# Optimization experiments

Hardware: AMD Instinct MI355X
Metric: run time of the kernel (lower is better)

Reference implementation:

```python
import jax, jax.numpy as jnp
import numpy as np

# Mamba-2 dims (from wrapper: d_model=hidden_size=2048, d_state=64, d_conv=4, expand=2, headdim=64)
D_MODEL = 2048
EXPAND = 2
HEADDIM = 64
D_STATE = 64
D_CONV = 4
D_INNER = EXPAND * D_MODEL            # 4096
NHEADS = D_INNER // HEADDIM           # 64
NGROUPS = 1                           # mamba_ssm default
CONV_DIM = D_INNER + 2 * NGROUPS * D_STATE          # 4224
D_IN_PROJ = 2 * D_INNER + 2 * NGROUPS * D_STATE + NHEADS  # 8384
BATCH = 1
SEQLEN = 1024
RMS_EPS = 1e-5


def setup_inputs() -> dict:
    key = jax.random.key(0)
    ks = jax.random.split(key, 8)
    x = jax.random.normal(ks[0], (BATCH, SEQLEN, D_MODEL), jnp.float32)
    W_in = jax.random.normal(ks[1], (D_IN_PROJ, D_MODEL), jnp.float32) * 0.02
    conv_w = jax.random.normal(ks[2], (CONV_DIM, D_CONV), jnp.float32) * 0.2
    conv_b = jnp.zeros((CONV_DIM,), jnp.float32)
    # dt_bias so that softplus(dt_raw + dt_bias) lands in a realistic dt range ~[1e-3, 5e-2]
    dt_bias = jax.random.uniform(ks[3], (NHEADS,), jnp.float32, -6.0, -3.0)
    # A = -exp(A_log), A_log init like mamba_ssm: A ~ Uniform(1, 16)
    A_log = jnp.log(1.0 + 15.0 * jax.random.uniform(ks[4], (NHEADS,), jnp.float32))
    D = jnp.ones((NHEADS,), jnp.float32)
    norm_w = jnp.ones((D_INNER,), jnp.float32)
    W_out = jax.random.normal(ks[5], (D_MODEL, D_INNER), jnp.float32) * 0.02
    return {"x": x, "W_in": W_in, "conv_w": conv_w, "conv_b": conv_b,
            "dt_bias": dt_bias, "A_log": A_log, "D": D, "norm_w": norm_w, "W_out": W_out}


def reference(x, W_in, conv_w, conv_b, dt_bias, A_log, D, norm_w, W_out):
    B, T, _ = x.shape
    # input projection -> [z | xBC | dt]
    zxbcdt = jnp.einsum('btd,pd->btp', x, W_in)
    z = zxbcdt[..., :D_INNER]                                  # [B,T,D_INNER] gate
    xBC = zxbcdt[..., D_INNER:D_INNER + CONV_DIM]              # [B,T,CONV_DIM]
    dt = jax.nn.softplus(zxbcdt[..., D_INNER + CONV_DIM:] + dt_bias)  # [B,T,H]
    # causal depthwise conv1d (kernel D_CONV) + SiLU
    xp = jnp.pad(xBC, ((0, 0), (D_CONV - 1, 0), (0, 0)))
    conv = conv_b + sum(xp[:, k:k + T, :] * conv_w[:, k] for k in range(D_CONV))
    xBC = jax.nn.silu(conv)
    xh = xBC[..., :D_INNER].reshape(B, T, NHEADS, HEADDIM)     # [B,T,H,P]
    Bm = xBC[..., D_INNER:D_INNER + D_STATE]                   # [B,T,N] (ngroups=1)
    Cm = xBC[..., D_INNER + D_STATE:]                          # [B,T,N]
    A = -jnp.exp(A_log)                                        # [H], negative
    dA = jnp.exp(dt * A)                                       # [B,T,H] decay per step

    def step(h, inp):
        # h: [B,H,P,N]
        dA_t, dt_t, B_t, x_t, C_t = inp
        h = h * dA_t[:, :, None, None] + jnp.einsum('bh,bn,bhp->bhpn', dt_t, B_t, x_t)
        y_t = jnp.einsum('bhpn,bn->bhp', h, C_t)
        return h, y_t

    h0 = jnp.zeros((B, NHEADS, HEADDIM, D_STATE), x.dtype)
    xs = (dA.transpose(1, 0, 2), dt.transpose(1, 0, 2), Bm.transpose(1, 0, 2),
          xh.transpose(1, 0, 2, 3), Cm.transpose(1, 0, 2))
    _, ys = jax.lax.scan(step, h0, xs)                         # ys: [T,B,H,P]
    y = ys.transpose(1, 0, 2, 3) + D[None, None, :, None] * xh  # skip term D*x
    y = y.reshape(B, T, D_INNER)
    # gated RMSNorm (norm_before_gate=False): norm(y * silu(z)) * weight
    y = y * jax.nn.silu(z)
    y = y * jax.lax.rsqrt(jnp.mean(y * y, axis=-1, keepdims=True) + RMS_EPS) * norm_w
    return jnp.einsum('bti,di->btd', y, W_out)
```

## Files before the change

### kernel.cpp

```cpp
#include <hip/hip_runtime.h>
#include <hip/hip_bf16.h>
#include <stdint.h>

#define SEQLEN   1024
#define DMODEL   2048
#define DINNER   4096
#define NHEADS   64
#define HEADDIM  64
#define DSTATE   64
#define CONVDIM  4224
#define DINPROJ  8384
#define RMS_EPS  1e-5f
#define CPAD     68

typedef __attribute__((ext_vector_type(8))) __bf16 bf16x8;
typedef __attribute__((ext_vector_type(4))) float f32x4;

__device__ __forceinline__ ushort f2bf(float f) {
    uint32_t u = __float_as_uint(f);
    u += 0x7FFFu + ((u >> 16) & 1u);
    return (ushort)(u >> 16);
}

__device__ __forceinline__ float silu(float a) { return a / (1.f + __expf(-a)); }

__device__ __forceinline__ void gload_lds16(const void* g, void* l) {
    __builtin_amdgcn_global_load_lds(
        (const __attribute__((address_space(1))) void*)g,
        (__attribute__((address_space(3))) void*)l, 16, 0, 0);
}

__global__ __launch_bounds__(256) void cvt3_kernel(
    const float* __restrict__ a, ushort* __restrict__ oa, int na4,
    const float* __restrict__ b, ushort* __restrict__ ob, int nb4,
    const float* __restrict__ c, ushort* __restrict__ oc, int nc4)
{
    int i = blockIdx.x * 256 + threadIdx.x;
    const float* src; ushort* dst;
    if (i < na4) { src = a; dst = oa; }
    else if (i < na4 + nb4) { i -= na4; src = b; dst = ob; }
    else { i -= na4 + nb4; if (i >= nc4) return; src = c; dst = oc; }
    float4 v = ((const float4*)src)[i];
    ushort4 o;
    o.x = f2bf(v.x); o.y = f2bf(v.y); o.z = f2bf(v.z); o.w = f2bf(v.w);
    ((ushort4*)dst)[i] = o;
}

__global__ __launch_bounds__(256, 4) void gemm4_bf16_nt(
    const __bf16* __restrict__ A, const __bf16* __restrict__ B,
    float* __restrict__ C, int M, int N, int K,
    int ntx, int nty, int nk, int ksteps, int swz)
{
    __shared__ __align__(16) __bf16 As[2][128 * 32];
    __shared__ __align__(16) __bf16 Bs[2][128 * 32];
    const int tid  = threadIdx.x;
    const int lane = tid & 63;
    const int wave = tid >> 6;
    const int wr = wave >> 1, wc = wave & 1;
    int id = blockIdx.x;
    if (swz) { int q = (ntx * nty * nk) >> 3; id = (id & 7) * q + (id >> 3); }
    const int kz  = id / (ntx * nty);
    const int rem = id % (ntx * nty);
    const int tx = rem / nty, ty = rem % nty;
    const int row0 = ty * 128, col0 = tx * 128;
    const int lr = lane & 15, lq = lane >> 4;
    const int rA = lane >> 2, jl = lane & 3;
    const int k0 = kz * ksteps * 32;

    const __bf16* srcA[2];
    const __bf16* srcB[2];
    int dstAB[2];
    #pragma unroll
    for (int e = 0; e < 2; ++e) {
        int r0 = (wave * 2 + e) * 16;
        int r  = r0 + rA;
        int jg = jl ^ ((rA >> 1) & 3);
        srcA[e] = A + (size_t)(row0 + r) * K + k0 + jg * 8;
        int gb = col0 + r; if (gb > N - 1) gb = N - 1;
        srcB[e] = B + (size_t)gb * K + k0 + jg * 8;
        dstAB[e] = r0 * 32;
    }

    f32x4 acc[4][4] = {};
    const int nt = ksteps;

#define STAGE(BUF)                                                            \
    _Pragma("unroll")                                                         \
    for (int e = 0; e < 2; ++e) {                                             \
        gload_lds16(srcA[e], &As[BUF][dstAB[e]]);                             \
        gload_lds16(srcB[e], &Bs[BUF][dstAB[e]]);                             \
        srcA[e] += 32; srcB[e] += 32;                                         \
    }

#define COMPUTE(BUF)                                                          \
    {                                                                         \
        bf16x8 af[4], bfr[4];                                                 \
        const int sl = (lq ^ ((lr >> 1) & 3)) * 8;                            \
        _Pragma("unroll")                                                     \
        for (int m = 0; m < 4; ++m) {                                         \
            int r = wr * 64 + m * 16 + lr;                                    \
            af[m] = *(const bf16x8*)(&As[BUF][r * 32 + sl]);                  \
        }                                                                     \
        _Pragma("unroll")                                                     \
        for (int n = 0; n < 4; ++n) {                                         \
            int r = wc * 64 + n * 16 + lr;                                    \
            bfr[n] = *(const bf16x8*)(&Bs[BUF][r * 32 + sl]);                 \
        }                                                                     \
        __builtin_amdgcn_s_setprio(1);                                        \
        _Pragma("unroll")                                                     \
        for (int m = 0; m < 4; ++m)                                           \
            _Pragma("unroll")                                                 \
            for (int n = 0; n < 4; ++n)                                       \
                acc[m][n] = __builtin_amdgcn_mfma_f32_16x16x32_bf16(af[m], bfr[n], acc[m][n], 0, 0, 0); \
        __builtin_amdgcn_s_setprio(0);                                        \
    }

    STAGE(0);
    asm volatile("s_waitcnt vmcnt(0)" ::: "memory");
    __builtin_amdgcn_s_barrier();
    asm volatile("" ::: "memory");

    for (int t = 0; t < nt; t += 2) {
        STAGE(1);
        COMPUTE(0);
        asm volatile("s_waitcnt vmcnt(0)" ::: "memory");
        __builtin_amdgcn_s_barrier();
        asm volatile("" ::: "memory");
        if (t + 2 < nt) { STAGE(0); }
        COMPUTE(1);
        asm volatile("s_waitcnt vmcnt(0)" ::: "memory");
        __builtin_amdgcn_s_barrier();
        asm volatile("" ::: "memory");
    }
#undef STAGE
#undef COMPUTE

    float* Co = C + (size_t)kz * M * N;
    #pragma unroll
    for (int m = 0; m < 4; ++m)
        #pragma unroll
        for (int n = 0; n < 4; ++n) {
            int col = col0 + wc * 64 + n * 16 + lr;
            if (col < N) {
                #pragma unroll
                for (int j = 0; j < 4; ++j) {
                    int row = row0 + wr * 64 + m * 16 + lq * 4 + j;
                    Co[(size_t)row * N + col] = acc[m][n][j];
                }
            }
        }
}

__global__ __launch_bounds__(256) void reduce4_scale_kernel(
    const float* __restrict__ p, const float* __restrict__ ssbuf,
    float* __restrict__ out, int n4)
{
    int i = blockIdx.x * 256 + threadIdx.x;
    if (i < n4) {
        int t = i >> 9;
        float sc = rsqrtf(ssbuf[t] * (1.f / DINNER) + RMS_EPS);
        float4 a = ((const float4*)p)[i];
        float4 b = ((const float4*)p)[i + n4];
        float4 c = ((const float4*)p)[i + 2 * (size_t)n4];
        float4 d = ((const float4*)p)[i + 3 * (size_t)n4];
        float4 o = {(a.x + b.x + c.x + d.x) * sc, (a.y + b.y + c.y + d.y) * sc,
                    (a.z + b.z + c.z + d.z) * sc, (a.w + b.w + c.w + d.w) * sc};
        ((float4*)out)[i] = o;
    }
}

__global__ __launch_bounds__(256) void chunk_intra_kernel(
    const float* __restrict__ zx, const float* __restrict__ conv_w,
    const float* __restrict__ conv_b, const float* __restrict__ dt_bias,
    const float* __restrict__ A_log,
    float* __restrict__ x_scan, float* __restrict__ Cb,
    float* __restrict__ yintra, float* __restrict__ Tc, float* __restrict__ Ssum)
{
    const int head  = blockIdx.x >> 4;
    const int chunk = blockIdx.x & 15;
    const int t0 = chunk * 64;
    const int tid = threadIdx.x;
    const int ty = tid >> 4, tx = tid & 15;
    const int lane = tid & 63, wv = tid >> 6;

    __shared__ __align__(16) float Xs [64][CPAD];
    __shared__ __align__(16) float BsT[64][CPAD];
    __shared__ __align__(16) float CsT[64][CPAD];
    __shared__ __align__(16) float GsT[64][CPAD];
    __shared__ float Sc[64], dts[64], ws[64];

    {
        const int c0 = head * 64 + tx * 4;
        float4 w0 = *(const float4*)&conv_w[(c0 + 0) * 4];
        float4 w1 = *(const float4*)&conv_w[(c0 + 1) * 4];
        float4 w2 = *(const float4*)&conv_w[(c0 + 2) * 4];
        float4 w3 = *(const float4*)&conv_w[(c0 + 3) * 4];
        float4 bv = *(const float4*)&conv_b[c0];
        #pragma unroll
        for (int pass = 0; pass < 4; ++pass) {
            int s = pass * 16 + ty;
            int gt = t0 + s;
            float4 r0 = {0,0,0,0}, r1 = {0,0,0,0}, r2 = {0,0,0,0}, r3;
            const float* base = zx + (size_t)gt * DINPROJ + DINNER + c0;
            if (gt >= 3) r0 = *(const float4*)(base - 3 * DINPROJ);
            if (gt >= 2) r1 = *(const float4*)(base - 2 * DINPROJ);
            if (gt >= 1) r2 = *(const float4*)(base - 1 * DINPROJ);
            r3 = *(const float4*)base;
            float4 o;
            o.x = silu(bv.x + r0.x*w0.x + r1.x*w0.y + r2.x*w0.z + r3.x*w0.w);
            o.y = silu(bv.y + r0.y*w1.x + r1.y*w1.y + r2.y*w1.z + r3.y*w1.w);
            o.z = silu(bv.z + r0.z*w2.x + r1.z*w2.y + r2.z*w2.z + r3.z*w2.w);
            o.w = silu(bv.w + r0.w*w3.x + r1.w*w3.y + r2.w*w3.z + r3.w*w3.w);
            *(float4*)&Xs[s][tx * 4] = o;
            *(float4*)&x_scan[(size_t)gt * DINNER + head * 64 + tx * 4] = o;
        }
    }

    #pragma unroll
    for (int k = 0; k < 4; ++k) {
        int n0 = wv * 16 + k * 4;
        int gt = t0 + lane;
        {
            float4 w0 = *(const float4*)&conv_w[(4096 + n0 + 0) * 4];
            float4 w1 = *(const float4*)&conv_w[(4096 + n0 + 1) * 4];
            float4 w2 = *(const float4*)&conv_w[(4096 + n0 + 2) * 4];
            float4 w3 = *(const float4*)&conv_w[(4096 + n0 + 3) * 4];
            float4 bv = *(const float4*)&conv_b[4096 + n0];
            float4 r0 = {0,0,0,0}, r1 = {0,0,0,0}, r2 = {0,0,0,0}, r3;
            const float* base = zx + (size_t)gt * DINPROJ + 8192 + n0;
            if (gt >= 3) r0 = *(const float4*)(base - 3 * DINPROJ);
            if (gt >= 2) r1 = *(const float4*)(base - 2 * DINPROJ);
            if (gt >= 1) r2 = *(const float4*)(base - 1 * DINPROJ);
            r3 = *(const float4*)base;
            BsT[n0+0][lane] = silu(bv.x + r0.x*w0.x + r1.x*w0.y + r2.x*w0.z + r3.x*w0.w);
            BsT[n0+1][lane] = silu(bv.y + r0.y*w1.x + r1.y*w1.y + r2.y*w1.z + r3.y*w1.w);
            BsT[n0+2][lane] = silu(bv.z + r0.z*w2.x + r1.z*w2.y + r2.z*w2.z + r3.z*w2.w);
            BsT[n0+3][lane] = silu(bv.w + r0.w*w3.x + r1.w*w3.y + r2.w*w3.z + r3.w*w3.w);
        }
        {
            float4 w0 = *(const float4*)&conv_w[(4160 + n0 + 0) * 4];
            float4 w1 = *(const float4*)&conv_w[(4160 + n0 + 1) * 4];
            float4 w2 = *(const float4*)&conv_w[(4160 + n0 + 2) * 4];
            float4 w3 = *(const float4*)&conv_w[(4160 + n0 + 3) * 4];
            float4 bv = *(const float4*)&conv_b[4160 + n0];
            float4 r0 = {0,0,0,0}, r1 = {0,0,0,0}, r2 = {0,0,0,0}, r3;
            const float* base = zx + (size_t)gt * DINPROJ + 8256 + n0;
            if (gt >= 3) r0 = *(const float4*)(base - 3 * DINPROJ);
            if (gt >= 2) r1 = *(const float4*)(base - 2 * DINPROJ);
            if (gt >= 1) r2 = *(const float4*)(base - 1 * DINPROJ);
            r3 = *(const float4*)base;
            float4 cv;
            cv.x = silu(bv.x + r0.x*w0.x + r1.x*w0.y + r2.x*w0.z + r3.x*w0.w);
            cv.y = silu(bv.y + r0.y*w1.x + r1.y*w1.y + r2.y*w1.z + r3.y*w1.w);
            cv.z = silu(bv.z + r0.z*w2.x + r1.z*w2.y + r2.z*w2.z + r3.z*w2.w);
            cv.w = silu(bv.w + r0.w*w3.x + r1.w*w3.y + r2.w*w3.z + r3.w*w3.w);
            CsT[n0+0][lane] = cv.x; CsT[n0+1][lane] = cv.y;
            CsT[n0+2][lane] = cv.z; CsT[n0+3][lane] = cv.w;
            if (head == 0) *(float4*)&Cb[(size_t)gt * 64 + n0] = cv;
        }
    }

    if (wv == 1) {
        float raw = zx[(size_t)(t0 + lane) * DINPROJ + 8320 + head] + dt_bias[head];
        float dt  = (raw > 20.f) ? raw : log1pf(__expf(raw));
        dts[lane] = dt;
        float v = dt * (-__expf(A_log[head]));
        #pragma unroll
        for (int off = 1; off < 64; off <<= 1) {
            float u = __shfl_up(v, off, 64);
            if (lane >= off) v += u;
        }
        Sc[lane] = v;
        Ssum[(t0 + lane) * 64 + head] = v;
    }
    __syncthreads();
    if (tid < 64) ws[tid] = dts[tid] * __expf(Sc[63] - Sc[tid]);

    float gacc[4][4] = {};
    for (int n = 0; n < 64; ++n) {
        float4 ci = *(const float4*)&CsT[n][ty * 4];
        float4 bs = *(const float4*)&BsT[n][tx * 4];
        gacc[0][0] += ci.x*bs.x; gacc[0][1] += ci.x*bs.y; gacc[0][2] += ci.x*bs.z; gacc[0][3] += ci.x*bs.w;
        gacc[1][0] += ci.y*bs.x; gacc[1][1] += ci.y*bs.y; gacc[1][2] += ci.y*bs.z; gacc[1][3] += ci.y*bs.w;
        gacc[2][0] += ci.z*bs.x; gacc[2][1] += ci.z*bs.y; gacc[2][2] += ci.z*bs.z; gacc[2][3] += ci.z*bs.w;
        gacc[3][0] += ci.w*bs.x; gacc[3][1] += ci.w*bs.y; gacc[3][2] += ci.w*bs.z; gacc[3][3] += ci.w*bs.w;
    }
    {
        float Si[4];
        #pragma unroll
        for (int di = 0; di < 4; ++di) Si[di] = Sc[ty * 4 + di];
        #pragma unroll
        for (int ds = 0; ds < 4; ++ds) {
            int s = tx * 4 + ds;
            float dw = dts[s], Ss_ = Sc[s];
            float4 g;
            g.x = (s <= ty*4+0) ? gacc[0][ds] * dw * __expf(Si[0] - Ss_) : 0.f;
            g.y = (s <= ty*4+1) ? gacc[1][ds] * dw * __expf(Si[1] - Ss_) : 0.f;
            g.z = (s <= ty*4+2) ? gacc[2][ds] * dw * __expf(Si[2] - Ss_) : 0.f;
            g.w = (s <= ty*4+3) ? gacc[3][ds] * dw * __expf(Si[3] - Ss_) : 0.f;
            *(float4*)&GsT[s][ty * 4] = g;
        }
    }
    __syncthreads();
    {
        int nn = wv * 16 + (lane >> 2);
        int s0 = (lane & 3) * 16;
        #pragma unroll
        for (int k = 0; k < 4; ++k) {
            float4 b = *(const float4*)&BsT[nn][s0 + k * 4];
            CsT[s0 + k*4 + 0][nn] = b.x;
            CsT[s0 + k*4 + 1][nn] = b.y;
            CsT[s0 + k*4 + 2][nn] = b.z;
            CsT[s0 + k*4 + 3][nn] = b.w;
        }
    }
    __syncthreads();

    float yacc[4][4] = {};
    float tacc[4][4] = {};
    for (int s = 0; s < 64; ++s) {
        float4 g  = *(const float4*)&GsT[s][ty * 4];
        float4 xp = *(const float4*)&Xs[s][tx * 4];
        float4 xq = *(const float4*)&Xs[s][ty * 4];
        float4 bn = *(const float4*)&CsT[s][tx * 4];
        float w = ws[s];
        yacc[0][0] += g.x*xp.x; yacc[0][1] += g.x*xp.y; yacc[0][2] += g.x*xp.z; yacc[0][3] += g.x*xp.w;
        yacc[1][0] += g.y*xp.x; yacc[1][1] += g.y*xp.y; yacc[1][2] += g.y*xp.z; yacc[1][3] += g.y*xp.w;
        yacc[2][0] += g.z*xp.x; yacc[2][1] += g.z*xp.y; yacc[2][2] += g.z*xp.z; yacc[2][3] += g.z*xp.w;
        yacc[3][0] += g.w*xp.x; yacc[3][1] += g.w*xp.y; yacc[3][2] += g.w*xp.z; yacc[3][3] += g.w*xp.w;
        float wx0 = xq.x * w, wx1 = xq.y * w, wx2 = xq.z * w, wx3 = xq.w * w;
        tacc[0][0] += wx0*bn.x; tacc[0][1] += wx0*bn.y; tacc[0][2] += wx0*bn.z; tacc[0][3] += wx0*bn.w;
        tacc[1][0] += wx1*bn.x; tacc[1][1] += wx1*bn.y; tacc[1][2] += wx1*bn.z; tacc[1][3] += wx1*bn.w;
        tacc[2][0] += wx2*bn.x; tacc[2][1] += wx2*bn.y; tacc[2][2] += wx2*bn.z; tacc[2][3] += wx2*bn.w;
        tacc[3][0] += wx3*bn.x; tacc[3][1] += wx3*bn.y; tacc[3][2] += wx3*bn.z; tacc[3][3] += wx3*bn.w;
    }
    #pragma unroll
    for (int di = 0; di < 4; ++di) {
        float4 yv = {yacc[di][0], yacc[di][1], yacc[di][2], yacc[di][3]};
        *(float4*)&yintra[(size_t)(t0 + ty*4 + di) * DINNER + head * 64 + tx * 4] = yv;
    }
    float* tcb = Tc + (size_t)(head * 16 + chunk) * 4096;
    #pragma unroll
    for (int dq = 0; dq < 4; ++dq) {
        float4 tv = {tacc[dq][0], tacc[dq][1], tacc[dq][2], tacc[dq][3]};
        *(float4*)&tcb[(ty*4 + dq) * 64 + tx * 4] = tv;
    }
}

__global__ __launch_bounds__(256) void chunk_state_kernel(
    float* __restrict__ Tc, const float* __restrict__ Ssum)
{
    const int head = blockIdx.x;
    const int tid = threadIdx.x;
    float h[16] = {};
    float* base = Tc + (size_t)head * 16 * 4096 + tid * 16;
    for (int c = 0; c < 16; ++c) {
        float Q = __expf(Ssum[(c * 64 + 63) * 64 + head]);
        float4* p = (float4*)(base + (size_t)c * 4096);
        #pragma unroll
        for (int v = 0; v < 4; ++v) {
            float4 t = p[v];
            float4 hold = {h[v*4], h[v*4+1], h[v*4+2], h[v*4+3]};
            h[v*4+0] = h[v*4+0] * Q + t.x;
            h[v*4+1] = h[v*4+1] * Q + t.y;
            h[v*4+2] = h[v*4+2] * Q + t.z;
            h[v*4+3] = h[v*4+3] * Q + t.w;
            p[v] = hold;
        }
    }
}

__global__ __launch_bounds__(256) void inter_combine_kernel(
    const float* __restrict__ Hpre, const float* __restrict__ Cb,
    const float* __restrict__ Ssum, const float* __restrict__ yintra,
    const float* __restrict__ x_scan, const float* __restrict__ zx,
    const float* __restrict__ Dv, const float* __restrict__ norm_w,
    ushort* __restrict__ ybf, float* __restrict__ ssbuf)
{
    const int head  = blockIdx.x >> 4;
    const int chunk = blockIdx.x & 15;
    const int t0 = chunk * 64;
    const int tid = threadIdx.x;
    const int ty = tid >> 4, tx = tid & 15;
    const int lane = tid & 63, wv = tid >> 6;

    __shared__ __align__(16) float HsT[64][CPAD];
    __shared__ __align__(16) float CsT[64][CPAD];
    __shared__ float Se[64];

    const float* hb = Hpre + (size_t)(head * 16 + chunk) * 4096;
    #pragma unroll
    for (int k = 0; k < 4; ++k) {
        int n0 = wv * 16 + k * 4;
        float4 h = *(const float4*)&hb[lane * 64 + n0];
        float4 c = *(const float4*)&Cb[(t0 + lane) * 64 + n0];
        HsT[n0][lane] = h.x; HsT[n0+1][lane] = h.y; HsT[n0+2][lane] = h.z; HsT[n0+3][lane] = h.w;
        CsT[n0][lane] = c.x; CsT[n0+1][lane] = c.y; CsT[n0+2][lane] = c.z; CsT[n0+3][lane] = c.w;
    }
    if (tid < 64) Se[tid] = __expf(Ssum[(t0 + tid) * 64 + head]);
    __syncthreads();

    float acc[4][4] = {};
    for (int n = 0; n < 64; ++n) {
        float4 ci = *(const float4*)&CsT[n][ty * 4];
        float4 hp = *(const float4*)&HsT[n][tx * 4];
        acc[0][0] += ci.x*hp.x; acc[0][1] += ci.x*hp.y; acc[0][2] += ci.x*hp.z; acc[0][3] += ci.x*hp.w;
        acc[1][0] += ci.y*hp.x; acc[1][1] += ci.y*hp.y; acc[1][2] += ci.y*hp.z; acc[1][3] += ci.y*hp.w;
        acc[2][0] += ci.z*hp.x; acc[2][1] += ci.z*hp.y; acc[2][2] += ci.z*hp.z; acc[2][3] += ci.z*hp.w;
        acc[3][0] += ci.w*hp.x; acc[3][1] += ci.w*hp.y; acc[3][2] += ci.w*hp.z; acc[3][3] += ci.w*hp.w;
    }

    const float Dh = Dv[head];
    const int col = head * 64 + tx * 4;
    float4 nw = *(const float4*)&norm_w[col];
    float ssp[4];
    #pragma unroll
    for (int di = 0; di < 4; ++di) {
        int t = t0 + ty * 4 + di;
        float se = Se[ty * 4 + di];
        float4 yi = *(const float4*)&yintra[(size_t)t * DINNER + col];
        float4 xh = *(const float4*)&x_scan[(size_t)t * DINNER + col];
        float4 zv = *(const float4*)&zx[(size_t)t * DINPROJ + col];
        float4 y;
        y.x = (acc[di][0] * se + yi.x + Dh * xh.x) * silu(zv.x);
        y.y = (acc[di][1] * se + yi.y + Dh * xh.y) * silu(zv.y);
        y.z = (acc[di][2] * se + yi.z + Dh * xh.z) * silu(zv.z);
        y.w = (acc[di][3] * se + yi.w + Dh * xh.w) * silu(zv.w);
        ssp[di] = y.x*y.x + y.y*y.y + y.z*y.z + y.w*y.w;
        ushort4 o;
        o.x = f2bf(y.x * nw.x); o.y = f2bf(y.y * nw.y);
        o.z = f2bf(y.z * nw.z); o.w = f2bf(y.w * nw.w);
        *(ushort4*)&ybf[(size_t)t * DINNER + col] = o;
    }
    #pragma unroll
    for (int di = 0; di < 4; ++di) {
        float s = ssp[di];
        s += __shfl_xor(s, 1, 64);
        s += __shfl_xor(s, 2, 64);
        s += __shfl_xor(s, 4, 64);
        s += __shfl_xor(s, 8, 64);
        if (tx == 0) atomicAdd(&ssbuf[t0 + ty * 4 + di], s);
    }
}

extern "C" void kernel_launch(void* const* d_in, const int* in_sizes, int n_in,
                              void* d_out, int out_size, void* d_ws, size_t ws_size,
                              hipStream_t stream)
{
    const float* x       = (const float*)d_in[0];
    const float* W_in    = (const float*)d_in[1];
    const float* conv_w  = (const float*)d_in[2];
    const float* conv_b  = (const float*)d_in[3];
    const float* dt_bias = (const float*)d_in[4];
    const float* A_log   = (const float*)d_in[5];
    const float* Dv      = (const float*)d_in[6];
    const float* norm_w  = (const float*)d_in[7];
    const float* W_out   = (const float*)d_in[8];
    float* out = (float*)d_out;

    char* ws = (char*)d_ws;
    const size_t OFF_WIN  = 0;
    const size_t OFF_WOUT = 34340864;
    const size_t OFF_XBF  = OFF_WOUT + 16777216;
    const size_t OFF_ZX   = OFF_XBF + 4194304;
    const size_t OFF_XSC  = OFF_ZX + 34340864;
    const size_t OFF_CB   = OFF_XSC + 16777216;
    const size_t OFF_SSB  = OFF_CB + 262144;
    const size_t OFF_YBF  = OFF_SSB + 4096;
    const size_t OFF_TC   = OFF_YBF + 8388608;
    const size_t OFF_SS   = OFF_TC + 16777216;

    ushort* WinBf  = (ushort*)(ws + OFF_WIN);
    ushort* WoutBf = (ushort*)(ws + OFF_WOUT);
    ushort* xBf    = (ushort*)(ws + OFF_XBF);
    float*  zxb    = (float*)(ws + OFF_ZX);
    float*  xsc    = (float*)(ws + OFF_XSC);
    float*  Cb     = (float*)(ws + OFF_CB);
    float*  ssbuf  = (float*)(ws + OFF_SSB);
    ushort* ybf    = (ushort*)(ws + OFF_YBF);
    float*  Tc     = (float*)(ws + OFF_TC);
    float*  Ssum   = (float*)(ws + OFF_SS);
    float*  yintra = (float*)(ws + OFF_WIN);
    float*  part   = (float*)(ws + OFF_WIN);

    const int nW4 = DINPROJ * DMODEL / 4;
    const int nO4 = DMODEL * DINNER / 4;
    const int nX4 = SEQLEN * DMODEL / 4;
    const int nAll = nW4 + nO4 + nX4;
    cvt3_kernel<<<(nAll + 255) / 256, 256, 0, stream>>>(
        W_in, WinBf, nW4, W_out, WoutBf, nO4, x, xBf, nX4);

    hipMemsetAsync(ssbuf, 0, SEQLEN * sizeof(float), stream);

    gemm4_bf16_nt<<<528, 256, 0, stream>>>(
        (const __bf16*)xBf, (const __bf16*)WinBf, zxb,
        SEQLEN, DINPROJ, DMODEL, 66, 8, 1, DMODEL / 32, 1);

    chunk_intra_kernel<<<1024, 256, 0, stream>>>(
        zxb, conv_w, conv_b, dt_bias, A_log, xsc, Cb, yintra, Tc, Ssum);

    chunk_state_kernel<<<64, 256, 0, stream>>>(Tc, Ssum);

    inter_combine_kernel<<<1024, 256, 0, stream>>>(
        Tc, Cb, Ssum, yintra, xsc, zxb, Dv, norm_w, ybf, ssbuf);

    gemm4_bf16_nt<<<512, 256, 0, stream>>>(
        (const __bf16*)ybf, (const __bf16*)WoutBf, part,
        SEQLEN, DMODEL, DINNER, 16, 8, 4, DINNER / 32 / 4, 1);

    reduce4_scale_kernel<<<(SEQLEN * DMODEL / 4 + 255) / 256, 256, 0, stream>>>(
        part, ssbuf, out, SEQLEN * DMODEL / 4);
}
```

Measured before the change: 203.9 us.

## Use bf16 MFMA for chunk-intra C·B, G·X and state-contribution matmuls

Replaces the scalar fp32 outer-product loops in chunk_intra_kernel with 16x16x32 bf16 MFMA instructions. Shared-memory tiles are stored as bf16 in layouts suited to MFMA operands, which removes the separate transpose pass and one barrier. The conv/SiLU for x is rewritten so each lane walks 16 timesteps with a sliding window. Launch bounds are raised to target more resident blocks. The cost is lower precision, since the intra-chunk products now round inputs to bf16, and the Tc output is written with scalar strided stores.

```diff
diff --git a/kernel.cpp b/kernel.cpp
--- a/kernel.cpp
+++ b/kernel.cpp
@@ -12,14 +12,20 @@
 #define DINPROJ  8384
 #define RMS_EPS  1e-5f
 #define CPAD     68
+#define LP       72
 
 typedef __attribute__((ext_vector_type(8))) __bf16 bf16x8;
+typedef __attribute__((ext_vector_type(8))) unsigned short us8;
 typedef __attribute__((ext_vector_type(4))) float f32x4;
 
 __device__ __forceinline__ ushort f2bf(float f) {
     uint32_t u = __float_as_uint(f);
     u += 0x7FFFu + ((u >> 16) & 1u);
     return (ushort)(u >> 16);
+}
+
+__device__ __forceinline__ float bf2f(ushort u) {
+    return __uint_as_float((uint32_t)u << 16);
 }
 
 __device__ __forceinline__ float silu(float a) { return a / (1.f + __expf(-a)); }
@@ -169,7 +175,7 @@
     }
 }
 
-__global__ __launch_bounds__(256) void chunk_intra_kernel(
+__global__ __launch_bounds__(256, 3) void chunk_intra_kernel(
     const float* __restrict__ zx, const float* __restrict__ conv_w,
     const float* __restrict__ conv_b, const float* __restrict__ dt_bias,
     const float* __restrict__ A_log,
@@ -180,40 +186,41 @@
     const int chunk = blockIdx.x & 15;
     const int t0 = chunk * 64;
     const int tid = threadIdx.x;
-    const int ty = tid >> 4, tx = tid & 15;
     const int lane = tid & 63, wv = tid >> 6;
-
-    __shared__ __align__(16) float Xs [64][CPAD];
-    __shared__ __align__(16) float BsT[64][CPAD];
-    __shared__ __align__(16) float CsT[64][CPAD];
-    __shared__ __align__(16) float GsT[64][CPAD];
+    const int lr = lane & 15, lq = lane >> 4;
+
+    __shared__ __align__(16) ushort XT [64 * LP];
+    __shared__ __align__(16) ushort Crm[64 * LP];
+    __shared__ __align__(16) ushort Brm[64 * LP];
+    __shared__ __align__(16) ushort BnT[64 * LP];
+    __shared__ __align__(16) ushort Grm[64 * LP];
     __shared__ float Sc[64], dts[64], ws[64];
 
     {
-        const int c0 = head * 64 + tx * 4;
-        float4 w0 = *(const float4*)&conv_w[(c0 + 0) * 4];
-        float4 w1 = *(const float4*)&conv_w[(c0 + 1) * 4];
-        float4 w2 = *(const float4*)&conv_w[(c0 + 2) * 4];
-        float4 w3 = *(const float4*)&conv_w[(c0 + 3) * 4];
-        float4 bv = *(const float4*)&conv_b[c0];
-        #pragma unroll
-        for (int pass = 0; pass < 4; ++pass) {
-            int s = pass * 16 + ty;
-            int gt = t0 + s;
-            float4 r0 = {0,0,0,0}, r1 = {0,0,0,0}, r2 = {0,0,0,0}, r3;
-            const float* base = zx + (size_t)gt * DINPROJ + DINNER + c0;
-            if (gt >= 3) r0 = *(const float4*)(base - 3 * DINPROJ);
-            if (gt >= 2) r1 = *(const float4*)(base - 2 * DINPROJ);
-            if (gt >= 1) r2 = *(const float4*)(base - 1 * DINPROJ);
-            r3 = *(const float4*)base;
-            float4 o;
-            o.x = silu(bv.x + r0.x*w0.x + r1.x*w0.y + r2.x*w0.z + r3.x*w0.w);
-            o.y = silu(bv.y + r0.y*w1.x + r1.y*w1.y + r2.y*w1.z + r3.y*w1.w);
-            o.z = silu(bv.z + r0.z*w2.x + r1.z*w2.y + r2.z*w2.z + r3.z*w2.w);
-            o.w = silu(bv.w + r0.w*w3.x + r1.w*w3.y + r2.w*w3.z + r3.w*w3.w);
-            *(float4*)&Xs[s][tx * 4] = o;
-            *(float4*)&x_scan[(size_t)gt * DINNER + head * 64 + tx * 4] = o;
-        }
+        const int p = lane;
+        const int c = head * 64 + p;
+        const float w0 = conv_w[c*4+0], w1 = conv_w[c*4+1];
+        const float w2 = conv_w[c*4+2], w3 = conv_w[c*4+3];
+        const float bia = conv_b[c];
+        const int gt0 = t0 + wv * 16;
+        const float* zc = zx + DINNER + c;
+        float xm3 = (gt0 >= 3) ? zc[(size_t)(gt0-3)*DINPROJ] : 0.f;
+        float xm2 = (gt0 >= 2) ? zc[(size_t)(gt0-2)*DINPROJ] : 0.f;
+        float xm1 = (gt0 >= 1) ? zc[(size_t)(gt0-1)*DINPROJ] : 0.f;
+        uint32_t pk[8];
+        #pragma unroll
+        for (int e = 0; e < 16; ++e) {
+            float xt = zc[(size_t)(gt0+e)*DINPROJ];
+            float s  = silu(bia + xm3*w0 + xm2*w1 + xm1*w2 + xt*w3);
+            x_scan[(size_t)(gt0+e)*DINNER + c] = s;
+            ushort b = f2bf(s);
+            if (e & 1) pk[e>>1] |= (uint32_t)b << 16; else pk[e>>1] = (uint32_t)b;
+            xm3 = xm2; xm2 = xm1; xm1 = xt;
+        }
+        int4 lo = { (int)pk[0], (int)pk[1], (int)pk[2], (int)pk[3] };
+        int4 hi = { (int)pk[4], (int)pk[5], (int)pk[6], (int)pk[7] };
+        *(int4*)&XT[p * LP + wv*16]     = lo;
+        *(int4*)&XT[p * LP + wv*16 + 8] = hi;
     }
 
     #pragma unroll
@@ -232,10 +239,15 @@
             if (gt >= 2) r1 = *(const float4*)(base - 2 * DINPROJ);
             if (gt >= 1) r2 = *(const float4*)(base - 1 * DINPROJ);
             r3 = *(const float4*)base;
-            BsT[n0+0][lane] = silu(bv.x + r0.x*w0.x + r1.x*w0.y + r2.x*w0.z + r3.x*w0.w);
-            BsT[n0+1][lane] = silu(bv.y + r0.y*w1.x + r1.y*w1.y + r2.y*w1.z + r3.y*w1.w);
-            BsT[n0+2][lane] = silu(bv.z + r0.z*w2.x + r1.z*w2.y + r2.z*w2.z + r3.z*w2.w);
-            BsT[n0+3][lane] = silu(bv.w + r0.w*w3.x + r1.w*w3.y + r2.w*w3.z + r3.w*w3.w);
+            ushort b0 = f2bf(silu(bv.x + r0.x*w0.x + r1.x*w0.y + r2.x*w0.z + r3.x*w0.w));
+            ushort b1 = f2bf(silu(bv.y + r0.y*w1.x + r1.y*w1.y + r2.y*w1.z + r3.y*w1.w));
+            ushort b2 = f2bf(silu(bv.z + r0.z*w2.x + r1.z*w2.y + r2.z*w2.z + r3.z*w2.w));
+            ushort b3 = f2bf(silu(bv.w + r0.w*w3.x + r1.w*w3.y + r2.w*w3.z + r3.w*w3.w));
+            uint2 pk = { (uint32_t)b0 | ((uint32_t)b1 << 16),
+                         (uint32_t)b2 | ((uint32_t)b3 << 16) };
+            *(uint2*)&Brm[lane * LP + n0] = pk;
+            BnT[(n0+0)*LP + lane] = b0; BnT[(n0+1)*LP + lane] = b1;
+            BnT[(n0+2)*LP + lane] = b2; BnT[(n0+3)*LP + lane] = b3;
         }
         {
             float4 w0 = *(const float4*)&conv_w[(4160 + n0 + 0) * 4];
@@ -254,8 +266,9 @@
             cv.y = silu(bv.y + r0.y*w1.x + r1.y*w1.y + r2.y*w1.z + r3.y*w1.w);
             cv.z = silu(bv.z + r0.z*w2.x + r1.z*w2.y + r2.z*w2.z + r3.z*w2.w);
             cv.w = silu(bv.w + r0.w*w3.x + r1.w*w3.y + r2.w*w3.z + r3.w*w3.w);
-            CsT[n0+0][lane] = cv.x; CsT[n0+1][lane] = cv.y;
-            CsT[n0+2][lane] = cv.z; CsT[n0+3][lane] = cv.w;
+            uint2 pk = { (uint32_t)f2bf(cv.x) | ((uint32_t)f2bf(cv.y) << 16),
+                         (uint32_t)f2bf(cv.z) | ((uint32_t)f2bf(cv.w) << 16) };
+            *(uint2*)&Crm[lane * LP + n0] = pk;
             if (head == 0) *(float4*)&Cb[(size_t)gt * 64 + n0] = cv;
         }
     }
@@ -276,74 +289,75 @@
     __syncthreads();
     if (tid < 64) ws[tid] = dts[tid] * __expf(Sc[63] - Sc[tid]);
 
-    float gacc[4][4] = {};
-    for (int n = 0; n < 64; ++n) {
-        float4 ci = *(const float4*)&CsT[n][ty * 4];
-        float4 bs = *(const float4*)&BsT[n][tx * 4];
-        gacc[0][0] += ci.x*bs.x; gacc[0][1] += ci.x*bs.y; gacc[0][2] += ci.x*bs.z; gacc[0][3] += ci.x*bs.w;
-        gacc[1][0] += ci.y*bs.x; gacc[1][1] += ci.y*bs.y; gacc[1][2] += ci.y*bs.z; gacc[1][3] += ci.y*bs.w;
-        gacc[2][0] += ci.z*bs.x; gacc[2][1] += ci.z*bs.y; gacc[2][2] += ci.z*bs.z; gacc[2][3] += ci.z*bs.w;
-        gacc[3][0] += ci.w*bs.x; gacc[3][1] += ci.w*bs.y; gacc[3][2] += ci.w*bs.z; gacc[3][3] += ci.w*bs.w;
+    const int i0 = wv * 16;
+    f32x4 gf[4] = {};
+    #pragma unroll
+    for (int kk = 0; kk < 2; ++kk) {
+        bf16x8 a = __builtin_bit_cast(bf16x8,
+            *(const us8*)&Crm[(i0 + lr) * LP + lq*8 + kk*32]);
+        #pragma unroll
+        for (int f = 0; f < 4; ++f) {
+            bf16x8 b = __builtin_bit_cast(bf16x8,
+                *(const us8*)&Brm[(f*16 + lr) * LP + lq*8 + kk*32]);
+            gf[f] = __builtin_amdgcn_mfma_f32_16x16x32_bf16(a, b, gf[f], 0, 0, 0);
+        }
     }
     {
         float Si[4];
         #pragma unroll
-        for (int di = 0; di < 4; ++di) Si[di] = Sc[ty * 4 + di];
-        #pragma unroll
-        for (int ds = 0; ds < 4; ++ds) {
-            int s = tx * 4 + ds;
+        for (int j = 0; j < 4; ++j) Si[j] = Sc[i0 + lq*4 + j];
+        #pragma unroll
+        for (int f = 0; f < 4; ++f) {
+            int s = f*16 + lr;
             float dw = dts[s], Ss_ = Sc[s];
-            float4 g;
-            g.x = (s <= ty*4+0) ? gacc[0][ds] * dw * __expf(Si[0] - Ss_) : 0.f;
-            g.y = (s <= ty*4+1) ? gacc[1][ds] * dw * __expf(Si[1] - Ss_) : 0.f;
-            g.z = (s <= ty*4+2) ? gacc[2][ds] * dw * __expf(Si[2] - Ss_) : 0.f;
-            g.w = (s <= ty*4+3) ? gacc[3][ds] * dw * __expf(Si[3] - Ss_) : 0.f;
-            *(float4*)&GsT[s][ty * 4] = g;
+            #pragma unroll
+            for (int j = 0; j < 4; ++j) {
+                int i = i0 + lq*4 + j;
+                float v = (s <= i) ? gf[f][j] * dw * __expf(Si[j] - Ss_) : 0.f;
+                Grm[i * LP + s] = f2bf(v);
+            }
         }
     }
     __syncthreads();
-    {
-        int nn = wv * 16 + (lane >> 2);
-        int s0 = (lane & 3) * 16;
-        #pragma unroll
-        for (int k = 0; k < 4; ++k) {
-            float4 b = *(const float4*)&BsT[nn][s0 + k * 4];
-            CsT[s0 + k*4 + 0][nn] = b.x;
-            CsT[s0 + k*4 + 1][nn] = b.y;
-            CsT[s0 + k*4 + 2][nn] = b.z;
-            CsT[s0 + k*4 + 3][nn] = b.w;
-        }
-    }
-    __syncthreads();
-
-    float yacc[4][4] = {};
-    float tacc[4][4] = {};
-    for (int s = 0; s < 64; ++s) {
-        float4 g  = *(const float4*)&GsT[s][ty * 4];
-        float4 xp = *(const float4*)&Xs[s][tx * 4];
-        float4 xq = *(const float4*)&Xs[s][ty * 4];
-        float4 bn = *(const float4*)&CsT[s][tx * 4];
-        float w = ws[s];
-        yacc[0][0] += g.x*xp.x; yacc[0][1] += g.x*xp.y; yacc[0][2] += g.x*xp.z; yacc[0][3] += g.x*xp.w;
-        yacc[1][0] += g.y*xp.x; yacc[1][1] += g.y*xp.y; yacc[1][2] += g.y*xp.z; yacc[1][3] += g.y*xp.w;
-        yacc[2][0] += g.z*xp.x; yacc[2][1] += g.z*xp.y; yacc[2][2] += g.z*xp.z; yacc[2][3] += g.z*xp.w;
-        yacc[3][0] += g.w*xp.x; yacc[3][1] += g.w*xp.y; yacc[3][2] += g.w*xp.z; yacc[3][3] += g.w*xp.w;
-        float wx0 = xq.x * w, wx1 = xq.y * w, wx2 = xq.z * w, wx3 = xq.w * w;
-        tacc[0][0] += wx0*bn.x; tacc[0][1] += wx0*bn.y; tacc[0][2] += wx0*bn.z; tacc[0][3] += wx0*bn.w;
-        tacc[1][0] += wx1*bn.x; tacc[1][1] += wx1*bn.y; tacc[1][2] += wx1*bn.z; tacc[1][3] += wx1*bn.w;
-        tacc[2][0] += wx2*bn.x; tacc[2][1] += wx2*bn.y; tacc[2][2] += wx2*bn.z; tacc[2][3] += wx2*bn.w;
-        tacc[3][0] += wx3*bn.x; tacc[3][1] += wx3*bn.y; tacc[3][2] += wx3*bn.z; tacc[3][3] += wx3*bn.w;
-    }
-    #pragma unroll
-    for (int di = 0; di < 4; ++di) {
-        float4 yv = {yacc[di][0], yacc[di][1], yacc[di][2], yacc[di][3]};
-        *(float4*)&yintra[(size_t)(t0 + ty*4 + di) * DINNER + head * 64 + tx * 4] = yv;
+
+    const int p0 = i0;
+    bf16x8 xa[2], xw[2];
+    #pragma unroll
+    for (int kk = 0; kk < 2; ++kk) {
+        us8 raw = *(const us8*)&XT[(p0 + lr) * LP + lq*8 + kk*32];
+        xa[kk] = __builtin_bit_cast(bf16x8, raw);
+        us8 sw;
+        #pragma unroll
+        for (int e = 0; e < 8; ++e) {
+            int s = lq*8 + kk*32 + e;
+            sw[e] = f2bf(bf2f(raw[e]) * ws[s]);
+        }
+        xw[kk] = __builtin_bit_cast(bf16x8, sw);
+    }
+    f32x4 yf[4] = {};
+    f32x4 tf[4] = {};
+    #pragma unroll
+    for (int kk = 0; kk < 2; ++kk) {
+        #pragma unroll
+        for (int f = 0; f < 4; ++f) {
+            bf16x8 gb = __builtin_bit_cast(bf16x8,
+                *(const us8*)&Grm[(f*16 + lr) * LP + lq*8 + kk*32]);
+            yf[f] = __builtin_amdgcn_mfma_f32_16x16x32_bf16(xa[kk], gb, yf[f], 0, 0, 0);
+            bf16x8 bb = __builtin_bit_cast(bf16x8,
+                *(const us8*)&BnT[(f*16 + lr) * LP + lq*8 + kk*32]);
+            tf[f] = __builtin_amdgcn_mfma_f32_16x16x32_bf16(xw[kk], bb, tf[f], 0, 0, 0);
+        }
     }
     float* tcb = Tc + (size_t)(head * 16 + chunk) * 4096;
     #pragma unroll
-    for (int dq = 0; dq < 4; ++dq) {
-        float4 tv = {tacc[dq][0], tacc[dq][1], tacc[dq][2], tacc[dq][3]};
-        *(float4*)&tcb[(ty*4 + dq) * 64 + tx * 4] = tv;
+    for (int f = 0; f < 4; ++f) {
+        int col = f*16 + lr;
+        int p   = p0 + lq*4;
+        float4 yv = {yf[f][0], yf[f][1], yf[f][2], yf[f][3]};
+        *(float4*)&yintra[(size_t)(t0 + col) * DINNER + head*64 + p] = yv;
+        #pragma unroll
+        for (int j = 0; j < 4; ++j)
+            tcb[(p + j) * 64 + col] = tf[f][j];
     }
 }
 
```

New measurement: 185.2 us. -9.2%, faster.
